# Kernel optimization log

Measured on AMD Instinct MI355X. Metric: run time of the kernel, lower is better.

Reference implementation:

```python
import jax, jax.numpy as jnp
import numpy as np

N_ATOMS = 50000
N_EDGES = 400000
EMB = 256
NUM_RBF = 50
NUM_GATES = 10
F_OUT = 128
BASE_CUTOFF = 0.0
OUTER_CUTOFF = 5.0


def _linear_params(k, din, dout):
    k1, k2 = jax.random.split(k)
    lim = 1.0 / np.sqrt(din)
    W = jax.random.uniform(k1, (din, dout), minval=-lim, maxval=lim, dtype=jnp.float32)
    b = jax.random.uniform(k2, (dout,), minval=-lim, maxval=lim, dtype=jnp.float32)
    return W, b


def setup_inputs() -> dict:
    key = jax.random.key(0)
    ks = jax.random.split(key, 16)
    z = jax.random.randint(ks[0], (N_ATOMS,), 0, 100)
    pos = jax.random.normal(ks[1], (N_ATOMS, 3), dtype=jnp.float32)
    batch = jnp.zeros((N_ATOMS,), dtype=jnp.int32)
    edge_index = jax.random.randint(ks[2], (2, N_EDGES), 0, N_ATOMS)
    edge_vec = jax.random.normal(ks[3], (N_EDGES, 3), dtype=jnp.float32)
    emb_table = jax.random.normal(ks[4], (100, EMB), dtype=jnp.float32)
    W_dist, b_dist = _linear_params(ks[5], NUM_RBF, EMB)
    W_dt, b_dt = _linear_params(ks[6], EMB + 6, EMB)
    W_ai, b_ai = _linear_params(ks[7], EMB, EMB)
    W_aj, b_aj = _linear_params(ks[8], EMB, EMB)
    W_gamma, b_gamma = _linear_params(ks[9], 3 * EMB, EMB)
    lim = 1.0 / np.sqrt(EMB)
    W_exp = jax.random.uniform(ks[10], (NUM_GATES, EMB, F_OUT), minval=-lim, maxval=lim, dtype=jnp.float32)
    b_exp = jax.random.uniform(ks[11], (NUM_GATES, F_OUT), minval=-lim, maxval=lim, dtype=jnp.float32)
    t_params = jax.random.normal(ks[12], (NUM_GATES,), dtype=jnp.float32) * 0.01
    return dict(z=z, pos=pos, batch=batch, edge_index=edge_index, edge_vec=edge_vec,
                emb_table=emb_table, W_dist=W_dist, b_dist=b_dist, W_dt=W_dt, b_dt=b_dt,
                W_ai=W_ai, b_ai=b_ai, W_aj=W_aj, b_aj=b_aj, W_gamma=W_gamma, b_gamma=b_gamma,
                W_exp=W_exp, b_exp=b_exp, t_params=t_params)


def _forward(z, edge_index, edge_vec, emb_table, W_dist, b_dist, W_dt, b_dt,
             W_ai, b_ai, W_aj, b_aj, W_gamma, b_gamma, W_exp, b_exp, t_params):
    x = emb_table[z]                                   # [N, EMB] embedding gather
    d = jnp.linalg.norm(edge_vec, axis=1)              # [E] edge distances
    # Gaussian RBF expansion (torchmd-net GaussianSmearing)
    offset = jnp.linspace(BASE_CUTOFF, OUTER_CUTOFF, NUM_RBF)
    coeff = -0.5 / (offset[1] - offset[0]) ** 2
    edge_attr = jnp.exp(coeff * (d[:, None] - offset[None, :]) ** 2)   # [E, NUM_RBF]
    # CosineCutoff with cutoff_lower == 0
    C = 0.5 * (jnp.cos(d * jnp.pi / OUTER_CUTOFF) + 1.0) * (d < OUTER_CUTOFF).astype(d.dtype)
    ev = edge_vec / d[:, None]                         # normalized edge vectors
    d_proj = (edge_attr @ W_dist + b_dist) * C[:, None]               # [E, EMB]
    feats = jnp.concatenate([d_proj, (d ** 2)[:, None], (d ** 3)[:, None], (d ** 4)[:, None],
                             jnp.sqrt(d)[:, None], jnp.log(d)[:, None], d[:, None]], axis=1)
    d_t = feats @ W_dt + b_dt                          # [E, EMB]
    a_i = x[edge_index[0]] @ W_ai + b_ai               # [E, EMB] gather + linear
    a_j = x[edge_index[1]] @ W_aj + b_aj
    gamma = jnp.concatenate([a_i, a_j, d_t], axis=1) @ W_gamma + b_gamma   # [E, EMB]
    # distance-based expert gate
    gate = jax.nn.softmax(1.0 / jnp.maximum(jnp.abs(d[:, None] - t_params[None, :]), 1e-8), axis=1)  # [E, G]
    edge_out = jnp.zeros((gamma.shape[0], F_OUT), gamma.dtype)
    for g in range(NUM_GATES):                          # small fixed expert loop
        edge_out = edge_out + gate[:, g:g + 1] * (gamma @ W_exp[g] + b_exp[g])
    # scatter to atoms
    atom_out = jax.ops.segment_sum(edge_out, edge_index[0], num_segments=N_ATOMS)   # [N, F_OUT]
    vec = jax.ops.segment_sum(ev[:, :, None] * edge_out[:, None, :], edge_index[0],
                              num_segments=N_ATOMS)                                  # [N, 3, F_OUT]
    return atom_out, vec


def reference(z, pos, batch, edge_index, edge_vec, emb_table, W_dist, b_dist, W_dt, b_dt,
              W_ai, b_ai, W_aj, b_aj, W_gamma, b_gamma, W_exp, b_exp, t_params):
    atom_out, vec = _forward(z, edge_index, edge_vec, emb_table, W_dist, b_dist, W_dt, b_dt,
                             W_ai, b_ai, W_aj, b_aj, W_gamma, b_gamma, W_exp, b_exp, t_params)
    return atom_out, vec, z, pos, batch
```

## Files before the change

### kernel.cpp

```cpp
#include <hip/hip_runtime.h>
#include <math.h>

typedef __bf16 bf16;
typedef __bf16 bf16x8 __attribute__((ext_vector_type(8)));
typedef float  f32x16 __attribute__((ext_vector_type(16)));

#define NATOMS 50000
#define NEDGES 400000
#define NG 10
#define NZ 100
#define BE 128
#define NBLK 3225
#define NLDSC 14
#define DELTA_F 0.10204081632653061f

#define OUT_VEC   6400000LL
#define OUT_Z     25600000LL
#define OUT_POS   25650000LL
#define OUT_BATCH 25800000LL

#define WS_M1   0LL
#define WS_M0   65536LL
#define WS_C0   78336LL
#define WS_M2   78592LL
#define WS_CC   80128LL
#define WS_AI   80384LL
#define WS_AJ   105984LL
#define WS_GI   131584LL
#define WS_GJ   157184LL
#define WS_HI   182784LL
#define WS_HJB  310784LL
#define WS_PTC  413184LL
#define WS_GT   451072LL
#define WS_EV   5404672LL
#define WS_EO   7055872LL
#define WS_I    33475072LL
#define I_CNT   0
#define I_START 50000
#define I_CUR   100000
#define I_CSR   150000
#define I_ZB    550000
#define I_ZC    550128
#define I_B2Z   550256
#define I_BSUM  553488
#define I_BOFF  553552
#define I_PERM  553616


__device__ __forceinline__ float dot256(const float* __restrict__ a,
                                        const float* __restrict__ B, int c)
{
    float s0 = 0, s1 = 0, s2 = 0, s3 = 0;
    for (int k = 0; k < 256; k += 4) {
        s0 += a[k]     * B[(k)     * 256 + c];
        s1 += a[k + 1] * B[(k + 1) * 256 + c];
        s2 += a[k + 2] * B[(k + 2) * 256 + c];
        s3 += a[k + 3] * B[(k + 3) * 256 + c];
    }
    return (s0 + s1) + (s2 + s3);
}

__device__ __forceinline__ unsigned pack2bf(float a, float b)
{
    union { __bf16 h; unsigned short u; } ca, cb;
    ca.h = (__bf16)a; cb.h = (__bf16)b;
    return (unsigned)ca.u | ((unsigned)cb.u << 16);
}


__global__ void kA(const float* __restrict__ W_dt, const float* __restrict__ b_dt,
                   const float* __restrict__ b_gamma, const float* __restrict__ Wg3,
                   float* __restrict__ M1, float* __restrict__ M2, float* __restrict__ cc,
                   const float* __restrict__ emb,
                   const float* __restrict__ W_ai, const float* __restrict__ b_ai,
                   const float* __restrict__ W_aj, const float* __restrict__ b_aj,
                   float* __restrict__ Ai, float* __restrict__ Aj,
                   const int* __restrict__ esrc, const int* __restrict__ edst,
                   const int* __restrict__ z,
                   int* __restrict__ cnt, int* __restrict__ zbins,
                   const float* __restrict__ pos, const int* __restrict__ batch,
                   float* __restrict__ out)
{
    const int r = blockIdx.x, tid = threadIdx.x;
    if (r < 263) {
        const float* a = (r < 262) ? (W_dt + (size_t)r * 256) : b_dt;
        float res = dot256(a, Wg3, tid);
        if (r == 262) res += b_gamma[tid];
        if (r < 256) M1[(size_t)r * 256 + tid] = res;
        else if (r < 262) M2[(size_t)(r - 256) * 256 + tid] = res;
        else cc[tid] = res;
    } else if (r < 463) {
        const int r2 = r - 263;
        const int zz = r2 % 100, side = r2 / 100;
        float res = dot256(emb + (size_t)zz * 256, side ? W_aj : W_ai, tid)
                  + (side ? b_aj[tid] : b_ai[tid]);
        (side ? Aj : Ai)[(size_t)zz * 256 + tid] = res;
    } else if (r < 2026) {
        __shared__ int h[NZ];
        for (int i = tid; i < NZ; i += 256) h[i] = 0;
        __syncthreads();
        const int e = (r - 463) * 256 + tid;
        if (e < NEDGES) {
            atomicAdd(&cnt[esrc[e]], 1);
            atomicAdd(&h[z[edst[e]]], 1);
        }
        __syncthreads();
        for (int i = tid; i < NZ; i += 256) if (h[i]) atomicAdd(&zbins[i], h[i]);
    } else {
        const int i = (r - 2026) * 256 + tid;
        if (i < NATOMS) {
            out[OUT_Z + i] = (float)z[i];
            out[OUT_BATCH + i] = (float)batch[i];
        }
        if (i < 3 * NATOMS) out[OUT_POS + i] = pos[i];
    }
}


__global__ void kB(const float* __restrict__ W_dist, const float* __restrict__ b_dist,
                   const float* __restrict__ M1, float* __restrict__ M0, float* __restrict__ c0,
                   const float* __restrict__ Ai, const float* __restrict__ Aj,
                   const float* __restrict__ Wg1, const float* __restrict__ Wg2,
                   float* __restrict__ Gi, float* __restrict__ Gj)
{
    const int r = blockIdx.x, c = threadIdx.x;
    if (r < 51) {
        const float* a = (r < 50) ? (W_dist + (size_t)r * 256) : b_dist;
        float res = dot256(a, M1, c);
        if (r < 50) M0[(size_t)r * 256 + c] = res; else c0[c] = res;
    } else {
        const int r2 = r - 51;
        const int zz = r2 % 100, side = r2 / 100;
        float res = side ? dot256(Aj + (size_t)zz * 256, Wg2, c)
                         : dot256(Ai + (size_t)zz * 256, Wg1, c);
        (side ? Gj : Gi)[(size_t)zz * 256 + c] = res;
    }
}


__global__ void kC(const float* __restrict__ Gi, const float* __restrict__ Gj,
                   const float* __restrict__ Wexp,
                   float* __restrict__ Hi, bf16* __restrict__ Hjb,
                   const float* __restrict__ M0, const float* __restrict__ M2,
                   const float* __restrict__ c0, const float* __restrict__ cc,
                   const float* __restrict__ b_exp, bf16* __restrict__ PTc)
{
    const int r = blockIdx.x;
    const int f = threadIdx.x;
    if (r < 1000) {
        const int zz = r / 10, g = r - zz * 10;
        const float* w  = Wexp + (size_t)g * 32768 + f;
        const float* gi = Gi + (size_t)zz * 256;
        const float* gj = Gj + (size_t)zz * 256;
        float a0=0,a1=0,a2=0,a3=0,b0=0,b1=0,b2=0,b3=0;
        for (int k = 0; k < 256; k += 4) {
            const float w0 = w[k*128], w1 = w[(k+1)*128], w2 = w[(k+2)*128], w3 = w[(k+3)*128];
            a0 += gi[k]*w0;   a1 += gi[k+1]*w1; a2 += gi[k+2]*w2; a3 += gi[k+3]*w3;
            b0 += gj[k]*w0;   b1 += gj[k+1]*w1; b2 += gj[k+2]*w2; b3 += gj[k+3]*w3;
        }
        Hi[(size_t)r * 128 + f] = (a0+a1)+(a2+a3);
        Hjb[(size_t)zz * 2048 + (g >> 3) * 1024 + f * 8 + (g & 7)] = (bf16)((b0+b1)+(b2+b3));
    } else {
        const int b = r - 1000;
        const int ck = b >> 4, kl = b & 15;
        const int k = ck * 16 + kl;
        float val = 0.f;
        if (k < 580) {
            const float* arow; int g; float bias = 0.f;
            if (k < 500)      { g = k / 50; arow = M0 + (size_t)(k - g * 50) * 256; }
            else if (k < 560) { const int jj = k - 500; g = jj / 6; arow = M2 + (size_t)(jj - g * 6) * 256; }
            else if (k < 570) { g = k - 560; arow = c0; }
            else              { g = k - 570; arow = cc; bias = b_exp[g * 128 + f]; }
            const float* w = Wexp + (size_t)g * 32768 + f;
            float s0=0,s1=0,s2=0,s3=0;
            for (int c2 = 0; c2 < 256; c2 += 4) {
                s0 += arow[c2]   * w[(c2)   * 128];
                s1 += arow[c2+1] * w[(c2+1) * 128];
                s2 += arow[c2+2] * w[(c2+2) * 128];
                s3 += arow[c2+3] * w[(c2+3) * 128];
            }
            val = (s0+s1)+(s2+s3) + bias;
        }
        PTc[(size_t)ck * 2048 + (kl >> 3) * 1024 + f * 8 + (kl & 7)] = (bf16)val;
    }
}


__global__ void kD1(const int* __restrict__ cnt, int* __restrict__ startp,
                    int* __restrict__ bsum)
{
    __shared__ int part[1024];
    const int tid = threadIdx.x;
    const int i = blockIdx.x * 1024 + tid;
    const int v = (i < NATOMS) ? cnt[i] : 0;
    part[tid] = v;
    __syncthreads();
    for (int off = 1; off < 1024; off <<= 1) {
        int t2 = part[tid];
        if (tid >= off) t2 += part[tid - off];
        __syncthreads();
        part[tid] = t2;
        __syncthreads();
    }
    if (i < NATOMS) startp[i] = part[tid] - v;
    if (tid == 1023) bsum[blockIdx.x] = part[1023];
}

__global__ void kD2(const int* __restrict__ bsum, int* __restrict__ boffs,
                    const int* __restrict__ zbins, int* __restrict__ zcursor,
                    int* __restrict__ blk2z)
{
    __shared__ int sc[256];
    const int tid = threadIdx.x;
    const int v = (tid < 49) ? bsum[tid] : 0;
    sc[tid] = v;
    __syncthreads();
    for (int off = 1; off < 64; off <<= 1) {
        int t2 = sc[tid];
        if (tid >= off) t2 += sc[tid - off];
        __syncthreads();
        sc[tid] = t2;
        __syncthreads();
    }
    if (tid < 49) boffs[tid] = sc[tid] - v;
    __syncthreads();
    const int pz = (tid < NZ) ? (((zbins[tid] + 127) >> 7) << 7) : 0;
    sc[tid] = pz;
    __syncthreads();
    for (int off = 1; off < 128; off <<= 1) {
        int t2 = sc[tid];
        if (tid >= off) t2 += sc[tid - off];
        __syncthreads();
        sc[tid] = t2;
        __syncthreads();
    }
    if (tid < NZ) {
        const int st = sc[tid] - pz;
        zcursor[tid] = st;
        for (int b = (st >> 7); b < (sc[tid] >> 7); ++b) blk2z[b] = tid;
    }
}

__global__ void kD3(const int* __restrict__ boffs, int* __restrict__ startp,
                    int* __restrict__ cursor)
{
    const int i = blockIdx.x * 1024 + threadIdx.x;
    if (i < NATOMS) {
        const int s2 = startp[i] + boffs[blockIdx.x];
        startp[i] = s2;
        cursor[i] = s2;
    }
}

#define ZF_EPB 1024
__global__ void __launch_bounds__(256) k_zfill(
    const int* __restrict__ edst, const int* __restrict__ z,
    const int* __restrict__ esrc,
    int* __restrict__ zcursor, int* __restrict__ cursor,
    int* __restrict__ perm, int* __restrict__ csr)
{
    __shared__ int h[NZ];
    __shared__ int base[NZ];
    const int t = threadIdx.x;
    for (int i = t; i < NZ; i += 256) h[i] = 0;
    __syncthreads();
    const int e0 = blockIdx.x * ZF_EPB;
    int rank[4], zb[4];
#pragma unroll
    for (int k2 = 0; k2 < 4; ++k2) {
        const int e = e0 + t + k2 * 256;
        if (e < NEDGES) { zb[k2] = z[edst[e]]; rank[k2] = atomicAdd(&h[zb[k2]], 1); }
        else zb[k2] = -1;
    }
    __syncthreads();
    for (int i = t; i < NZ; i += 256) base[i] = h[i] ? atomicAdd(&zcursor[i], h[i]) : 0;
    __syncthreads();
#pragma unroll
    for (int k2 = 0; k2 < 4; ++k2) {
        if (zb[k2] >= 0) {
            const int e = e0 + t + k2 * 256;
            const int pos = base[zb[k2]] + rank[k2];
            perm[pos] = e;
            const int p2 = atomicAdd(&cursor[esrc[e]], 1);
            csr[p2] = pos;
        }
    }
}


__device__ __forceinline__ float coeff(int k, const unsigned* Gp, const float* gate,
                                       const float* sv, float C)
{
    if (k < 500) {
        const int g = k / 50, rb = k - g * 50;
        const unsigned w = Gp[rb >> 1];
        const unsigned bits = (rb & 1) ? (w & 0xffff0000u) : (w << 16);
        return gate[g] * __uint_as_float(bits);
    } else if (k < 560) {
        const int jj = k - 500;
        return gate[jj / 6] * sv[jj - (jj / 6) * 6];
    } else if (k < 570) {
        return C * gate[k - 560];
    } else if (k < 580) {
        return gate[k - 570];
    }
    return 0.0f;
}

__global__ void __launch_bounds__(256, 2) k_edge(
    const float* __restrict__ edge_vec,
    const int* __restrict__ perm, const int* __restrict__ blk2z,
    const float* __restrict__ tpar,
    const bf16* __restrict__ PTc, const bf16* __restrict__ Hjb,
    float* __restrict__ gates_ws, float* __restrict__ evb, bf16* __restrict__ eo)
{
    __shared__ __align__(16) bf16 Bs[(NLDSC + 1) * 2048];

    const int t    = threadIdx.x;
    const int wid  = t >> 6;
    const int lane = t & 63;
    const int er   = lane & 31;
    const int kh   = lane >> 5;
    const bool khb = (kh != 0);
    const int base = blockIdx.x * BE;
    const int pid  = base + wid * 32 + er;

    if (perm[base] < 0) return;

    const int zb  = blk2z[blockIdx.x];
    const int eid = perm[pid];

    const float4* PTc4 = (const float4*)PTc;
    float4 stg[NLDSC];
#pragma unroll
    for (int i = 0; i < NLDSC; ++i) stg[i] = PTc4[t + i * 256];
    const float4 hv = ((const float4*)(Hjb + (size_t)zb * 2048))[t];

    float gate[NG], sv[6];
    float d = 1.0f, C = 0.0f, vx = 0.f, vy = 0.f, vz = 0.f;
    if (eid >= 0) {
        vx = edge_vec[eid * 3]; vy = edge_vec[eid * 3 + 1]; vz = edge_vec[eid * 3 + 2];
        d = sqrtf(vx * vx + vy * vy + vz * vz);
        C = (d < 5.0f) ? 0.5f * (__cosf(d * 0.6283185307179586f) + 1.0f) : 0.0f;
        float m = -3.0e38f;
#pragma unroll
        for (int g = 0; g < NG; ++g) {
            float r = 1.0f / fmaxf(fabsf(d - tpar[g]), 1e-8f);
            gate[g] = r; m = fmaxf(m, r);
        }
        float ss = 0.f;
#pragma unroll
        for (int g = 0; g < NG; ++g) { float ex = __expf(gate[g] - m); gate[g] = ex; ss += ex; }
        const float inv = 1.0f / ss;
#pragma unroll
        for (int g = 0; g < NG; ++g) gate[g] *= inv;
        const float d2 = d * d;
        sv[0] = d2; sv[1] = d2 * d; sv[2] = d2 * d2;
        sv[3] = sqrtf(d); sv[4] = __logf(d); sv[5] = d;
    } else {
#pragma unroll
        for (int g = 0; g < NG; ++g) gate[g] = 0.f;
#pragma unroll
        for (int m2 = 0; m2 < 6; ++m2) sv[m2] = 0.f;
    }

    unsigned Gp[25];
#pragma unroll
    for (int p = 0; p < 25; ++p) {
        const float t0 = d - (float)(2 * p) * DELTA_F;
        const float t1 = t0 - DELTA_F;
        const float g0 = C * __expf(-48.02f * t0 * t0);
        const float g1 = C * __expf(-48.02f * t1 * t1);
        Gp[p] = pack2bf(g0, g1);
    }

    if (kh == 0 && eid >= 0) {
        float* gw = gates_ws + (size_t)pid * 12;
#pragma unroll
        for (int g = 0; g < NG; ++g) gw[g] = gate[g];
        const float invd = 1.0f / d;
        *(float4*)(evb + (size_t)pid * 4) =
            make_float4(vx * invd, vy * invd, vz * invd, 0.0f);
    }

    {
        float4* dst = (float4*)Bs;
#pragma unroll
        for (int i = 0; i < NLDSC; ++i) dst[t + i * 256] = stg[i];
        dst[t + NLDSC * 256] = hv;
    }
    __syncthreads();

    f32x16 acc0 = {}, acc1 = {}, acc2 = {}, acc3 = {};
    const int lanoff = kh * 1024 + er * 8;
    const bf16* Lp = Bs + lanoff;
    const bf16* Gb = PTc + lanoff;

#define MFMA4(AV, B0, B1, B2, B3) do { \
        acc0 = __builtin_amdgcn_mfma_f32_32x32x16_bf16(AV, B0, acc0, 0, 0, 0); \
        acc1 = __builtin_amdgcn_mfma_f32_32x32x16_bf16(AV, B1, acc1, 0, 0, 0); \
        acc2 = __builtin_amdgcn_mfma_f32_32x32x16_bf16(AV, B2, acc2, 0, 0, 0); \
        acc3 = __builtin_amdgcn_mfma_f32_32x32x16_bf16(AV, B3, acc3, 0, 0, 0); \
    } while (0)
#define LDB(P, V0, V1, V2, V3) \
        const bf16x8 V0 = *(const bf16x8*)(P); \
        const bf16x8 V1 = *(const bf16x8*)((P) + 256); \
        const bf16x8 V2 = *(const bf16x8*)((P) + 512); \
        const bf16x8 V3 = *(const bf16x8*)((P) + 768);

    {
        bf16x8 av;
#pragma unroll
        for (int j = 0; j < 8; ++j) {
            const float va = gate[j];
            const float vb = (j < 2) ? gate[8 + j] : 0.0f;
            av[j] = (bf16)(khb ? vb : va);
        }
        LDB(Lp + NLDSC * 2048, b0, b1, b2, b3);
        MFMA4(av, b0, b1, b2, b3);
    }

    bf16x8 c0, c1, c2, c3, n0, n1, n2, n3;
    {
        const bf16* bp = Gb + NLDSC * 2048;
        c0 = *(const bf16x8*)(bp);       c1 = *(const bf16x8*)(bp + 256);
        c2 = *(const bf16x8*)(bp + 512); c3 = *(const bf16x8*)(bp + 768);
    }
    {
        const bf16* bp = Gb + (NLDSC + 1) * 2048;
        n0 = *(const bf16x8*)(bp);       n1 = *(const bf16x8*)(bp + 256);
        n2 = *(const bf16x8*)(bp + 512); n3 = *(const bf16x8*)(bp + 768);
    }

#pragma unroll
    for (int ks = 0; ks < NLDSC; ++ks) {
        bf16x8 av;
#pragma unroll
        for (int j = 0; j < 8; ++j) {
            const float va = coeff(ks * 16 + j,     Gp, gate, sv, C);
            const float vb = coeff(ks * 16 + 8 + j, Gp, gate, sv, C);
            av[j] = (bf16)(khb ? vb : va);
        }
        LDB(Lp + ks * 2048, b0, b1, b2, b3);
        MFMA4(av, b0, b1, b2, b3);
    }

#pragma unroll
    for (int ks = NLDSC; ks < 37; ++ks) {
        const bf16x8 m0 = c0, m1 = c1, m2 = c2, m3 = c3;
        c0 = n0; c1 = n1; c2 = n2; c3 = n3;
        if (ks + 2 <= 36) {
            const bf16* bp = Gb + (size_t)(ks + 2) * 2048;
            n0 = *(const bf16x8*)(bp);       n1 = *(const bf16x8*)(bp + 256);
            n2 = *(const bf16x8*)(bp + 512); n3 = *(const bf16x8*)(bp + 768);
        }
        bf16x8 av;
#pragma unroll
        for (int j = 0; j < 8; ++j) {
            const float va = coeff(ks * 16 + j,     Gp, gate, sv, C);
            const float vb = coeff(ks * 16 + 8 + j, Gp, gate, sv, C);
            av[j] = (bf16)(khb ? vb : va);
        }
        MFMA4(av, m0, m1, m2, m3);
    }
#undef MFMA4
#undef LDB

    bf16* eor = eo + (size_t)(base + wid * 32) * 128 + er;
#pragma unroll
    for (int r = 0; r < 16; ++r) {
        const int crow = (r & 3) + 8 * (r >> 2) + 4 * kh;
        bf16* p = eor + (size_t)crow * 128;
        p[0]  = (bf16)acc0[r];
        p[32] = (bf16)acc1[r];
        p[64] = (bf16)acc2[r];
        p[96] = (bf16)acc3[r];
    }
}


__global__ void __launch_bounds__(256) k_gather(
    const bf16* __restrict__ eo, const float* __restrict__ evb,
    const float* __restrict__ gates_ws,
    const int* __restrict__ startp, const int* __restrict__ cnt,
    const int* __restrict__ csr, const int* __restrict__ zarr,
    const float* __restrict__ Hi, float* __restrict__ out)
{
    __shared__ float gsum[4][48];
    const int wloc = threadIdx.x >> 6;
    const int atom = blockIdx.x * 4 + wloc;
    const int lane = threadIdx.x & 63;
    if (atom >= NATOMS) return;
    const int s = startp[atom], len = cnt[atom];
    const unsigned* eo32 = (const unsigned*)eo;
    const float4* ev4 = (const float4*)evb;

    const int comp = lane / 10;
    const int gidx = lane - comp * 10;
    const bool gl = (lane < 40);
    float gacc = 0.0f;

    float a0 = 0, a1 = 0, v00 = 0, v01 = 0, v10 = 0, v11 = 0, v20 = 0, v21 = 0;

#define ACCE(PID, EV, U) do { \
        const float evc = (comp == 1) ? EV.x : (comp == 2) ? EV.y : (comp == 3) ? EV.z : 1.0f; \
        if (gl) gacc += evc * gates_ws[(size_t)(PID) * 12 + gidx]; \
        const float y0 = __uint_as_float((U) << 16); \
        const float y1 = __uint_as_float((U) & 0xffff0000u); \
        a0 += y0; a1 += y1; \
        v00 += EV.x * y0; v01 += EV.x * y1; \
        v10 += EV.y * y0; v11 += EV.y * y1; \
        v20 += EV.z * y0; v21 += EV.z * y1; \
    } while (0)

    int i = 0;
    for (; i + 4 <= len; i += 4) {
        const int p0 = csr[s + i],     p1 = csr[s + i + 1];
        const int p2 = csr[s + i + 2], p3 = csr[s + i + 3];
        const float4 e0 = ev4[p0], e1 = ev4[p1], e2 = ev4[p2], e3 = ev4[p3];
        const unsigned u0 = eo32[(size_t)p0 * 64 + lane];
        const unsigned u1 = eo32[(size_t)p1 * 64 + lane];
        const unsigned u2 = eo32[(size_t)p2 * 64 + lane];
        const unsigned u3 = eo32[(size_t)p3 * 64 + lane];
        ACCE(p0, e0, u0);
        ACCE(p1, e1, u1);
        ACCE(p2, e2, u2);
        ACCE(p3, e3, u3);
    }
    for (; i < len; ++i) {
        const int p0 = csr[s + i];
        const float4 e0 = ev4[p0];
        const unsigned u0 = eo32[(size_t)p0 * 64 + lane];
        ACCE(p0, e0, u0);
    }
#undef ACCE

    if (gl) gsum[wloc][comp * 10 + gidx] = gacc;

    const float* Hrow = Hi + (size_t)zarr[atom] * 1280;
#pragma unroll
    for (int g = 0; g < NG; ++g) {
        const float gs = gsum[wloc][g];
        const float e0 = gsum[wloc][10 + g];
        const float e1 = gsum[wloc][20 + g];
        const float e2 = gsum[wloc][30 + g];
        const float2 h2 = *(const float2*)(Hrow + g * 128 + 2 * lane);
        a0  += gs * h2.x;  a1  += gs * h2.y;
        v00 += e0 * h2.x;  v01 += e0 * h2.y;
        v10 += e1 * h2.x;  v11 += e1 * h2.y;
        v20 += e2 * h2.x;  v21 += e2 * h2.y;
    }
    float* ao = out + (size_t)atom * 128;
    *(float2*)(ao + 2 * lane) = make_float2(a0, a1);
    float* vp = out + OUT_VEC + (size_t)atom * 384;
    *(float2*)(vp + 2 * lane)       = make_float2(v00, v01);
    *(float2*)(vp + 128 + 2 * lane) = make_float2(v10, v11);
    *(float2*)(vp + 256 + 2 * lane) = make_float2(v20, v21);
}


extern "C" void kernel_launch(void* const* d_in, const int* in_sizes, int n_in,
                              void* d_out, int out_size, void* d_ws, size_t ws_size,
                              hipStream_t stream)
{
    const int*   z        = (const int*)d_in[0];
    const float* pos      = (const float*)d_in[1];
    const int*   batch    = (const int*)d_in[2];
    const int*   esrc     = (const int*)d_in[3];
    const int*   edst     = esrc + NEDGES;
    const float* edge_vec = (const float*)d_in[4];
    const float* emb      = (const float*)d_in[5];
    const float* W_dist   = (const float*)d_in[6];
    const float* b_dist   = (const float*)d_in[7];
    const float* W_dt     = (const float*)d_in[8];
    const float* b_dt     = (const float*)d_in[9];
    const float* W_ai     = (const float*)d_in[10];
    const float* b_ai     = (const float*)d_in[11];
    const float* W_aj     = (const float*)d_in[12];
    const float* b_aj     = (const float*)d_in[13];
    const float* W_gamma  = (const float*)d_in[14];
    const float* b_gamma  = (const float*)d_in[15];
    const float* W_exp    = (const float*)d_in[16];
    const float* b_exp    = (const float*)d_in[17];
    const float* tpar     = (const float*)d_in[18];

    float* out = (float*)d_out;
    float* W   = (float*)d_ws;

    const float* Wg1 = W_gamma;
    const float* Wg2 = W_gamma + 256 * 256;
    const float* Wg3 = W_gamma + 512 * 256;

    float* M1 = W + WS_M1;
    float* M0 = W + WS_M0;
    float* c0 = W + WS_C0;
    float* M2 = W + WS_M2;
    float* cc = W + WS_CC;
    float* Ai = W + WS_AI;
    float* Aj = W + WS_AJ;
    float* Gi = W + WS_GI;
    float* Gj = W + WS_GJ;
    float* Hi = W + WS_HI;
    bf16*  Hjb = (bf16*)(W + WS_HJB);
    bf16*  PTc = (bf16*)(W + WS_PTC);
    float* gates = W + WS_GT;
    float* evb   = W + WS_EV;
    bf16*  eo    = (bf16*)(W + WS_EO);
    int*   I     = (int*)(W + WS_I);
    int* cnt    = I + I_CNT;
    int* startp = I + I_START;
    int* cursor = I + I_CUR;
    int* csr    = I + I_CSR;
    int* zbins  = I + I_ZB;
    int* zcur   = I + I_ZC;
    int* b2z    = I + I_B2Z;
    int* bsum   = I + I_BSUM;
    int* boffs  = I + I_BOFF;
    int* perm   = I + I_PERM;

    hipMemsetAsync(cnt, 0, NATOMS * sizeof(int), stream);
    hipMemsetAsync(zbins, 0, 128 * sizeof(int), stream);
    hipMemsetAsync(perm, 0xFF, (size_t)NBLK * BE * sizeof(int), stream);
    hipMemsetAsync(Hjb, 0, 100 * 2048 * sizeof(bf16), stream);

    kA<<<2613, 256, 0, stream>>>(W_dt, b_dt, b_gamma, Wg3, M1, M2, cc,
                                 emb, W_ai, b_ai, W_aj, b_aj, Ai, Aj,
                                 esrc, edst, z, cnt, zbins, pos, batch, out);
    kB<<<251, 256, 0, stream>>>(W_dist, b_dist, M1, M0, c0, Ai, Aj, Wg1, Wg2, Gi, Gj);
    kC<<<1592, 128, 0, stream>>>(Gi, Gj, W_exp, Hi, Hjb, M0, M2, c0, cc, b_exp, PTc);
    kD1<<<49, 1024, 0, stream>>>(cnt, startp, bsum);
    kD2<<<1, 256, 0, stream>>>(bsum, boffs, zbins, zcur, b2z);
    kD3<<<49, 1024, 0, stream>>>(boffs, startp, cursor);
    k_zfill<<<(NEDGES + ZF_EPB - 1) / ZF_EPB, 256, 0, stream>>>(edst, z, esrc, zcur, cursor, perm, csr);

    k_edge<<<NBLK, 256, 0, stream>>>(edge_vec, perm, b2z, tpar, PTc, Hjb, gates, evb, eo);
    k_gather<<<(NATOMS + 3) / 4, 256, 0, stream>>>(eo, evb, gates, startp, cnt, csr, z, Hi, out);
}
```

Before: 259.6 us.

## Fuse setup kernels, replace memsets with one init kernel, register-tile expert projection

Replaces four hipMemsetAsync calls with a single grid-stride init kernel. Merges the weight-precompute kernels with the first and second scan stages, so independent work shares a launch. This cuts the launch count from roughly ten to seven. The Hi/Hjb expert projection now stages 8 rows of Gi/Gj in shared memory per block and reuses each W_exp load across 8 accumulators instead of 2, which reduces redundant weight reads. kBD1 launches 1024-thread blocks where most threads idle for the dot-product part. kCD2 also zeroes blk2z explicitly.

New measurement: 254.7 us, median of 2. No clear change (-1.9%).

```diff
diff --git a/kernel.cpp b/kernel.cpp
--- a/kernel.cpp
+++ b/kernel.cpp
@@ -68,6 +68,18 @@
 }
 
 
+__global__ void k0(int* __restrict__ cnt, int* __restrict__ zbins,
+                   int* __restrict__ perm, int* __restrict__ hjz)
+{
+    const int i = blockIdx.x * 256 + threadIdx.x;
+    const int stride = gridDim.x * 256;
+    for (int j = i; j < NATOMS; j += stride) cnt[j] = 0;
+    if (i < 128) zbins[i] = 0;
+    for (int j = i; j < NBLK * BE; j += stride) perm[j] = -1;
+    for (int j = i; j < 102400; j += stride) hjz[j] = 0;
+}
+
+
 __global__ void kA(const float* __restrict__ W_dt, const float* __restrict__ b_dt,
                    const float* __restrict__ b_gamma, const float* __restrict__ Wg3,
                    float* __restrict__ M1, float* __restrict__ M2, float* __restrict__ cc,
@@ -117,51 +129,90 @@
 }
 
 
-__global__ void kB(const float* __restrict__ W_dist, const float* __restrict__ b_dist,
-                   const float* __restrict__ M1, float* __restrict__ M0, float* __restrict__ c0,
-                   const float* __restrict__ Ai, const float* __restrict__ Aj,
-                   const float* __restrict__ Wg1, const float* __restrict__ Wg2,
-                   float* __restrict__ Gi, float* __restrict__ Gj)
-{
-    const int r = blockIdx.x, c = threadIdx.x;
-    if (r < 51) {
-        const float* a = (r < 50) ? (W_dist + (size_t)r * 256) : b_dist;
-        float res = dot256(a, M1, c);
-        if (r < 50) M0[(size_t)r * 256 + c] = res; else c0[c] = res;
+__global__ void __launch_bounds__(1024) kBD1(
+    const float* __restrict__ W_dist, const float* __restrict__ b_dist,
+    const float* __restrict__ M1, float* __restrict__ M0, float* __restrict__ c0,
+    const float* __restrict__ Ai, const float* __restrict__ Aj,
+    const float* __restrict__ Wg1, const float* __restrict__ Wg2,
+    float* __restrict__ Gi, float* __restrict__ Gj,
+    const int* __restrict__ cnt, int* __restrict__ startp, int* __restrict__ bsum)
+{
+    const int r = blockIdx.x, tid = threadIdx.x;
+    if (r < 251) {
+        if (tid < 256) {
+            const int c = tid;
+            if (r < 51) {
+                const float* a = (r < 50) ? (W_dist + (size_t)r * 256) : b_dist;
+                float res = dot256(a, M1, c);
+                if (r < 50) M0[(size_t)r * 256 + c] = res; else c0[c] = res;
+            } else {
+                const int r2 = r - 51;
+                const int zz = r2 % 100, side = r2 / 100;
+                float res = side ? dot256(Aj + (size_t)zz * 256, Wg2, c)
+                                 : dot256(Ai + (size_t)zz * 256, Wg1, c);
+                (side ? Gj : Gi)[(size_t)zz * 256 + c] = res;
+            }
+        }
     } else {
-        const int r2 = r - 51;
-        const int zz = r2 % 100, side = r2 / 100;
-        float res = side ? dot256(Aj + (size_t)zz * 256, Wg2, c)
-                         : dot256(Ai + (size_t)zz * 256, Wg1, c);
-        (side ? Gj : Gi)[(size_t)zz * 256 + c] = res;
-    }
-}
-
-
-__global__ void kC(const float* __restrict__ Gi, const float* __restrict__ Gj,
-                   const float* __restrict__ Wexp,
-                   float* __restrict__ Hi, bf16* __restrict__ Hjb,
-                   const float* __restrict__ M0, const float* __restrict__ M2,
-                   const float* __restrict__ c0, const float* __restrict__ cc,
-                   const float* __restrict__ b_exp, bf16* __restrict__ PTc)
+        __shared__ int part[1024];
+        const int b = r - 251;
+        const int i = b * 1024 + tid;
+        const int v = (i < NATOMS) ? cnt[i] : 0;
+        part[tid] = v;
+        __syncthreads();
+        for (int off = 1; off < 1024; off <<= 1) {
+            int t2 = part[tid];
+            if (tid >= off) t2 += part[tid - off];
+            __syncthreads();
+            part[tid] = t2;
+            __syncthreads();
+        }
+        if (i < NATOMS) startp[i] = part[tid] - v;
+        if (tid == 1023) bsum[b] = part[1023];
+    }
+}
+
+
+__global__ void __launch_bounds__(128) kCD2(
+    const float* __restrict__ Gi, const float* __restrict__ Gj,
+    const float* __restrict__ Wexp,
+    float* __restrict__ Hi, bf16* __restrict__ Hjb,
+    const float* __restrict__ M0, const float* __restrict__ M2,
+    const float* __restrict__ c0, const float* __restrict__ cc,
+    const float* __restrict__ b_exp, bf16* __restrict__ PTc,
+    const int* __restrict__ bsum, int* __restrict__ boffs,
+    const int* __restrict__ zbins, int* __restrict__ zcursor,
+    int* __restrict__ blk2z)
 {
     const int r = blockIdx.x;
     const int f = threadIdx.x;
-    if (r < 1000) {
-        const int zz = r / 10, g = r - zz * 10;
-        const float* w  = Wexp + (size_t)g * 32768 + f;
-        const float* gi = Gi + (size_t)zz * 256;
-        const float* gj = Gj + (size_t)zz * 256;
-        float a0=0,a1=0,a2=0,a3=0,b0=0,b1=0,b2=0,b3=0;
-        for (int k = 0; k < 256; k += 4) {
-            const float w0 = w[k*128], w1 = w[(k+1)*128], w2 = w[(k+2)*128], w3 = w[(k+3)*128];
-            a0 += gi[k]*w0;   a1 += gi[k+1]*w1; a2 += gi[k+2]*w2; a3 += gi[k+3]*w3;
-            b0 += gj[k]*w0;   b1 += gj[k+1]*w1; b2 += gj[k+2]*w2; b3 += gj[k+3]*w3;
-        }
-        Hi[(size_t)r * 128 + f] = (a0+a1)+(a2+a3);
-        Hjb[(size_t)zz * 2048 + (g >> 3) * 1024 + f * 8 + (g & 7)] = (bf16)((b0+b1)+(b2+b3));
-    } else {
-        const int b = r - 1000;
+    if (r < 250) {
+        __shared__ float Gs[8][256];
+        const int g  = r / 25;
+        const int z0 = (r % 25) * 4;
+        for (int idx = f; idx < 8 * 256; idx += 128) {
+            const int row = idx >> 8, k = idx & 255;
+            const int zi = row >> 1, side = row & 1;
+            Gs[row][k] = side ? Gj[(size_t)(z0 + zi) * 256 + k]
+                              : Gi[(size_t)(z0 + zi) * 256 + k];
+        }
+        __syncthreads();
+        const float* w = Wexp + (size_t)g * 32768 + f;
+        float acc[8] = {};
+#pragma unroll 4
+        for (int k = 0; k < 256; ++k) {
+            const float wv = w[k * 128];
+#pragma unroll
+            for (int rr = 0; rr < 8; ++rr) acc[rr] += Gs[rr][k] * wv;
+        }
+#pragma unroll
+        for (int zi = 0; zi < 4; ++zi) {
+            const int zz = z0 + zi;
+            Hi[((size_t)zz * 10 + g) * 128 + f] = acc[zi * 2];
+            Hjb[(size_t)zz * 2048 + (g >> 3) * 1024 + f * 8 + (g & 7)] = (bf16)acc[zi * 2 + 1];
+        }
+    } else if (r < 842) {
+        const int b = r - 250;
         const int ck = b >> 4, kl = b & 15;
         const int k = ck * 16 + kl;
         float val = 0.f;
@@ -182,62 +233,38 @@
             val = (s0+s1)+(s2+s3) + bias;
         }
         PTc[(size_t)ck * 2048 + (kl >> 3) * 1024 + f * 8 + (kl & 7)] = (bf16)val;
-    }
-}
-
-
-__global__ void kD1(const int* __restrict__ cnt, int* __restrict__ startp,
-                    int* __restrict__ bsum)
-{
-    __shared__ int part[1024];
-    const int tid = threadIdx.x;
-    const int i = blockIdx.x * 1024 + tid;
-    const int v = (i < NATOMS) ? cnt[i] : 0;
-    part[tid] = v;
-    __syncthreads();
-    for (int off = 1; off < 1024; off <<= 1) {
-        int t2 = part[tid];
-        if (tid >= off) t2 += part[tid - off];
-        __syncthreads();
-        part[tid] = t2;
-        __syncthreads();
-    }
-    if (i < NATOMS) startp[i] = part[tid] - v;
-    if (tid == 1023) bsum[blockIdx.x] = part[1023];
-}
-
-__global__ void kD2(const int* __restrict__ bsum, int* __restrict__ boffs,
-                    const int* __restrict__ zbins, int* __restrict__ zcursor,
-                    int* __restrict__ blk2z)
-{
-    __shared__ int sc[256];
-    const int tid = threadIdx.x;
-    const int v = (tid < 49) ? bsum[tid] : 0;
-    sc[tid] = v;
-    __syncthreads();
-    for (int off = 1; off < 64; off <<= 1) {
-        int t2 = sc[tid];
-        if (tid >= off) t2 += sc[tid - off];
-        __syncthreads();
-        sc[tid] = t2;
-        __syncthreads();
-    }
-    if (tid < 49) boffs[tid] = sc[tid] - v;
-    __syncthreads();
-    const int pz = (tid < NZ) ? (((zbins[tid] + 127) >> 7) << 7) : 0;
-    sc[tid] = pz;
-    __syncthreads();
-    for (int off = 1; off < 128; off <<= 1) {
-        int t2 = sc[tid];
-        if (tid >= off) t2 += sc[tid - off];
-        __syncthreads();
-        sc[tid] = t2;
-        __syncthreads();
-    }
-    if (tid < NZ) {
-        const int st = sc[tid] - pz;
-        zcursor[tid] = st;
-        for (int b = (st >> 7); b < (sc[tid] >> 7); ++b) blk2z[b] = tid;
+    } else {
+        __shared__ int sc[128];
+        const int tid = f;
+        const int v = (tid < 49) ? bsum[tid] : 0;
+        sc[tid] = v;
+        __syncthreads();
+        for (int off = 1; off < 64; off <<= 1) {
+            int t2 = sc[tid];
+            if (tid >= off) t2 += sc[tid - off];
+            __syncthreads();
+            sc[tid] = t2;
+            __syncthreads();
+        }
+        if (tid < 49) boffs[tid] = sc[tid] - v;
+        __syncthreads();
+        const int pz = (tid < NZ) ? (((zbins[tid] + 127) >> 7) << 7) : 0;
+        sc[tid] = pz;
+        __syncthreads();
+        for (int off = 1; off < 128; off <<= 1) {
+            int t2 = sc[tid];
+            if (tid >= off) t2 += sc[tid - off];
+            __syncthreads();
+            sc[tid] = t2;
+            __syncthreads();
+        }
+        for (int b = tid; b < NBLK; b += 128) blk2z[b] = 0;
+        __syncthreads();
+        if (tid < NZ) {
+            const int st = sc[tid] - pz;
+            zcursor[tid] = st;
+            for (int b = (st >> 7); b < (sc[tid] >> 7); ++b) blk2z[b] = tid;
+        }
     }
 }
 
@@ -618,18 +645,14 @@
     int* boffs  = I + I_BOFF;
     int* perm   = I + I_PERM;
 
-    hipMemsetAsync(cnt, 0, NATOMS * sizeof(int), stream);
-    hipMemsetAsync(zbins, 0, 128 * sizeof(int), stream);
-    hipMemsetAsync(perm, 0xFF, (size_t)NBLK * BE * sizeof(int), stream);
-    hipMemsetAsync(Hjb, 0, 100 * 2048 * sizeof(bf16), stream);
-
+    k0<<<1024, 256, 0, stream>>>(cnt, zbins, perm, (int*)Hjb);
     kA<<<2613, 256, 0, stream>>>(W_dt, b_dt, b_gamma, Wg3, M1, M2, cc,
                                  emb, W_ai, b_ai, W_aj, b_aj, Ai, Aj,
                                  esrc, edst, z, cnt, zbins, pos, batch, out);
-    kB<<<251, 256, 0, stream>>>(W_dist, b_dist, M1, M0, c0, Ai, Aj, Wg1, Wg2, Gi, Gj);
-    kC<<<1592, 128, 0, stream>>>(Gi, Gj, W_exp, Hi, Hjb, M0, M2, c0, cc, b_exp, PTc);
-    kD1<<<49, 1024, 0, stream>>>(cnt, startp, bsum);
-    kD2<<<1, 256, 0, stream>>>(bsum, boffs, zbins, zcur, b2z);
+    kBD1<<<300, 1024, 0, stream>>>(W_dist, b_dist, M1, M0, c0, Ai, Aj, Wg1, Wg2,
+                                   Gi, Gj, cnt, startp, bsum);
+    kCD2<<<843, 128, 0, stream>>>(Gi, Gj, W_exp, Hi, Hjb, M0, M2, c0, cc, b_exp,
+                                  PTc, bsum, boffs, zbins, zcur, b2z);
     kD3<<<49, 1024, 0, stream>>>(boffs, startp, cursor);
     k_zfill<<<(NEDGES + ZF_EPB - 1) / ZF_EPB, 256, 0, stream>>>(edst, z, esrc, zcur, cursor, perm, csr);
 
```
